# Kernel optimization log

Hardware: AMD Instinct MI355X
Metric: run time of the kernel (lower is better)

## Reference

```python
import jax, jax.numpy as jnp
import numpy as np

NUM_GRAPHS = 256
BN_EPS = 1e-5


def _bn(x, gamma, beta):
    # torch BatchNorm1d training-mode forward: biased batch stats
    m = jnp.mean(x, axis=0)
    v = jnp.mean((x - m) ** 2, axis=0)
    return (x - m) * jax.lax.rsqrt(v + BN_EPS) * gamma + beta


def setup_inputs() -> dict:
    key = jax.random.key(0)
    ks = jax.random.split(key, 12)
    N, D, S = 400000, 128, 64
    h = jax.random.normal(ks[0], (N, D), dtype=jnp.float32)
    sub = jax.random.normal(ks[1], (N, S), dtype=jnp.float32)
    batch = jnp.sort(jax.random.randint(ks[2], (N,), 0, NUM_GRAPHS, dtype=jnp.int32))
    sc = lambda fan_in: 1.0 / np.sqrt(fan_in)
    return {
        "h": h, "sub": sub, "batch": batch,
        # sub_enhance: Linear(S, D) + BN(D) + ReLU
        "W1": jax.random.uniform(ks[3], (S, D), jnp.float32, -sc(S), sc(S)),
        "b1": jnp.zeros((D,), jnp.float32),
        "g1": jnp.ones((D,), jnp.float32),
        "be1": jnp.zeros((D,), jnp.float32),
        # gate: Linear(2D, D) + Sigmoid
        "Wg": jax.random.uniform(ks[4], (2 * D, D), jnp.float32, -sc(2 * D), sc(2 * D)),
        "bg": jnp.zeros((D,), jnp.float32),
        # score_mlp: Linear(2D, D) + BN + ReLU + Linear(D, 1)
        "Ws1": jax.random.uniform(ks[5], (2 * D, D), jnp.float32, -sc(2 * D), sc(2 * D)),
        "bs1": jnp.zeros((D,), jnp.float32),
        "g2": jnp.ones((D,), jnp.float32),
        "be2": jnp.zeros((D,), jnp.float32),
        "Ws2": jax.random.uniform(ks[6], (D, 1), jnp.float32, -sc(D), sc(D)),
        "bs2": jnp.zeros((1,), jnp.float32),
        "mix": jnp.float32(0.5),
    }


def reference(h, sub, batch, W1, b1, g1, be1, Wg, bg, Ws1, bs1, g2, be2, Ws2, bs2, mix):
    G = NUM_GRAPHS
    # counts per graph, guard against empty segments
    counts = jax.ops.segment_sum(jnp.ones_like(batch, jnp.float32), batch, num_segments=G)
    counts = jnp.maximum(counts, 1.0)[:, None]  # [G,1]

    sub_enhanced = jax.nn.relu(_bn(sub @ W1 + b1, g1, be1))  # [N,D]
    gate_weight = jax.nn.sigmoid(jnp.concatenate([h, sub_enhanced], axis=1) @ Wg + bg)
    h_fused = h + gate_weight * sub_enhanced  # [N,D]

    graph_mean = jax.ops.segment_sum(h, batch, num_segments=G) / counts  # [G,D]
    h_sq_mean = jax.ops.segment_sum(h * h, batch, num_segments=G) / counts
    graph_std = jnp.sqrt(jnp.maximum(h_sq_mean - graph_mean ** 2, 1e-8))
    h_dev = (h - graph_mean[batch]) / (graph_std[batch] + 1e-8)  # [N,D]

    z = jax.nn.relu(_bn(jnp.concatenate([h_fused, h_dev], axis=1) @ Ws1 + bs1, g2, be2))
    score_logit = z @ Ws2 + bs2  # [N,1]

    # scatter_softmax over batch segments
    seg_max = jax.ops.segment_max(score_logit, batch, num_segments=G)  # [G,1]
    e = jnp.exp(score_logit - seg_max[batch])
    denom = jax.ops.segment_sum(e, batch, num_segments=G)[batch]
    score = e / denom  # [N,1]

    weighted_fused = jax.ops.segment_sum(h_fused * score, batch, num_segments=G)  # [G,D]
    weighted_orig = graph_mean
    alpha = jax.nn.sigmoid(mix)
    return alpha * weighted_fused + (1.0 - alpha) * weighted_orig
```

## Files before the change

### kernel.cpp

```cpp
#include <hip/hip_runtime.h>

#define DD 128
#define SS 64
#define GG 256
#define LTDA 264
#define LTDS 72

typedef short short8 __attribute__((ext_vector_type(8)));
typedef float f32x4 __attribute__((ext_vector_type(4)));

__device__ __forceinline__ unsigned short f2bf(float x) {
  unsigned u = __float_as_uint(x);
  u += 0x7FFFu + ((u >> 16) & 1u);
  return (unsigned short)(u >> 16);
}
__device__ __forceinline__ float bf2f(unsigned short b) {
  return __uint_as_float(((unsigned)b) << 16);
}
__device__ __forceinline__ unsigned pkbf(float lo, float hi) {
  unsigned r;
  asm("v_cvt_pk_bf16_f32 %0, %1, %2" : "=v"(r) : "v"(lo), "v"(hi));
  return r;
}
__device__ __forceinline__ float fsig(float x) {
  return __builtin_amdgcn_rcpf(1.f + __expf(-x));
}

__device__ __forceinline__ void stage8k(const unsigned short* __restrict__ g,
                                        unsigned short* l, int tid) {
  int wave = tid >> 6;
  const unsigned* gp = (const unsigned*)g;
  unsigned* lp = (unsigned*)l;
  __builtin_amdgcn_global_load_lds(
      (const __attribute__((address_space(1))) unsigned*)(gp + tid * 4),
      (__attribute__((address_space(3))) unsigned*)(lp + wave * 256), 16, 0, 0);
  __builtin_amdgcn_global_load_lds(
      (const __attribute__((address_space(1))) unsigned*)(gp + 1024 + tid * 4),
      (__attribute__((address_space(3))) unsigned*)(lp + 1024 + wave * 256), 16, 0, 0);
}

__device__ __forceinline__ void mfma8(const unsigned short* __restrict__ Abase,
                                      int astride,
                                      const unsigned short* __restrict__ wst,
                                      int k0, int m16, int quad, int mts,
                                      int nts, f32x4 acc[2][4]) {
  short8 af[2];
  af[0] = *(const short8*)(Abase + (size_t)((mts + 0) * 16 + m16) * astride + k0 + quad * 8);
  af[1] = *(const short8*)(Abase + (size_t)((mts + 1) * 16 + m16) * astride + k0 + quad * 8);
  short8 bf[4];
#pragma unroll
  for (int ni = 0; ni < 4; ++ni) {
    int n = (nts + ni) * 16 + m16;
    int s = (quad + (n >> 1)) & 3;
    bf[ni] = *(const short8*)(wst + n * 32 + s * 8);
  }
#pragma unroll
  for (int mi = 0; mi < 2; ++mi)
#pragma unroll
    for (int ni = 0; ni < 4; ++ni)
      acc[mi][ni] = __builtin_amdgcn_mfma_f32_16x16x32_bf16(af[mi], bf[ni],
                                                            acc[mi][ni], 0, 0, 0);
}

__device__ __forceinline__ void mfma8t(const unsigned short* __restrict__ wst,
                                       const unsigned short* __restrict__ Abase,
                                       int k0, int m16, int quad, int mts,
                                       int nts, f32x4 acc[4][2]) {
  short8 wfr[4];
#pragma unroll
  for (int mi = 0; mi < 4; ++mi) {
    int ch = (mts + mi) * 16 + m16;
    int s = (quad + (ch >> 1)) & 3;
    wfr[mi] = *(const short8*)(wst + ch * 32 + s * 8);
  }
  short8 xf[2];
#pragma unroll
  for (int ni = 0; ni < 2; ++ni) {
    int row = (nts + ni) * 16 + m16;
    xf[ni] = *(const short8*)(Abase + (size_t)row * LTDA + k0 + quad * 8);
  }
#pragma unroll
  for (int mi = 0; mi < 4; ++mi)
#pragma unroll
    for (int ni = 0; ni < 2; ++ni)
      acc[mi][ni] = __builtin_amdgcn_mfma_f32_16x16x32_bf16(wfr[mi], xf[ni],
                                                            acc[mi][ni], 0, 0, 0);
}

__global__ void w_prep(const float* __restrict__ W1, const float* __restrict__ Wg,
                       const float* __restrict__ Ws1, unsigned short* __restrict__ w1t,
                       unsigned short* __restrict__ wgt, unsigned short* __restrict__ ws1t) {
  int cb = blockIdx.x;
  const float* W;
  unsigned short* out;
  int kb;
  if (cb < 2) { W = W1; out = w1t; kb = cb; }
  else if (cb < 10) { W = Wg; out = wgt; kb = cb - 2; }
  else { W = Ws1; out = ws1t; kb = cb - 10; }
  out += (size_t)kb * 4096;
  int i = threadIdx.x;
#pragma unroll
  for (int t = 0; t < 2; ++t) {
    int u = i * 2 + t;
    int n = u >> 2, s = u & 3;
    int kc = (s - (n >> 1)) & 3;
    int kbase = kb * 32 + kc * 8;
    unsigned short* o = out + u * 8;
#pragma unroll
    for (int j = 0; j < 8; ++j) o[j] = f2bf(W[(size_t)(kbase + j) * DD + n]);
  }
}

__global__ __launch_bounds__(256, 6) void k1_bn(
    const float* __restrict__ sub, const unsigned short* __restrict__ w1t,
    const float* __restrict__ b1, float* __restrict__ bn1s,
    float* __restrict__ bn1q) {
  __shared__ unsigned short subbuf[64][LTDS];
  __shared__ unsigned short wstage[2][4096];
  __shared__ float bn1l[256];
  int tid = threadIdx.x;
  int row0 = blockIdx.x * 64;
  bn1l[tid] = 0.f;
  for (int i = tid; i < 1024; i += 256) {
    int r = i >> 4, c = (i & 15) * 4;
    float4 v = *(const float4*)&sub[(size_t)(row0 + r) * SS + c];
    uint2 uu;
    uu.x = pkbf(v.x, v.y);
    uu.y = pkbf(v.z, v.w);
    *(uint2*)&subbuf[r][c] = uu;
  }
  stage8k(w1t, &wstage[0][0], tid);
  stage8k(w1t + 4096, &wstage[1][0], tid);
  __syncthreads();
  int lane = tid & 63, wave = tid >> 6;
  int m16 = lane & 15, quad = lane >> 4;
  int mts = 2 * (wave & 1), nts = 4 * (wave >> 1);
  f32x4 acc[2][4];
#pragma unroll
  for (int mi = 0; mi < 2; ++mi)
#pragma unroll
    for (int ni = 0; ni < 4; ++ni) acc[mi][ni] = (f32x4){0.f, 0.f, 0.f, 0.f};
  mfma8(&subbuf[0][0], LTDS, &wstage[0][0], 0, m16, quad, mts, nts, acc);
  mfma8(&subbuf[0][0], LTDS, &wstage[1][0], 32, m16, quad, mts, nts, acc);
#pragma unroll
  for (int ni = 0; ni < 4; ++ni) {
    int col = (nts + ni) * 16 + m16;
    float b1c = b1[col];
    float s = 0.f, q = 0.f;
#pragma unroll
    for (int mi = 0; mi < 2; ++mi)
#pragma unroll
      for (int r = 0; r < 4; ++r) {
        float x = acc[mi][ni][r] + b1c;
        s += x;
        q += x * x;
      }
    s += __shfl_down(s, 32); s += __shfl_down(s, 16);
    q += __shfl_down(q, 32); q += __shfl_down(q, 16);
    if (lane < 16) {
      atomicAdd(&bn1l[col], s);
      atomicAdd(&bn1l[128 + col], q);
    }
  }
  __syncthreads();
  if (tid < 128) {
    atomicAdd(&bn1s[tid], bn1l[tid]);
    atomicAdd(&bn1q[tid], bn1l[128 + tid]);
  }
}

__global__ __launch_bounds__(256, 8) void k1_graph(
    const float* __restrict__ h, const int* __restrict__ batch,
    float* __restrict__ gsum, float* __restrict__ gsq,
    float* __restrict__ counts, int N) {
  __shared__ int bc[256];
  int tid = threadIdx.x;
  int row0 = blockIdx.x * 256;
  {
    int row = row0 + tid;
    bc[tid] = (row < N) ? batch[row] : -1;
  }
  __syncthreads();
  int stripe = tid >> 5, c4 = (tid & 31) * 4;
  float sx = 0, sy = 0, sz = 0, sw = 0, qx = 0, qy = 0, qz = 0, qw = 0, cnt = 0;
  int gcur = -1;
  float4 vbuf[4];
  bool vval[4];
#pragma unroll
  for (int j = 0; j < 4; ++j) {
    int r = stripe + 8 * j;
    vval[j] = bc[r] >= 0;
    if (vval[j]) vbuf[j] = *(const float4*)&h[(size_t)(row0 + r) * DD + c4];
  }
#pragma unroll 1
  for (int mit = 0; mit < 8; ++mit) {
#pragma unroll
    for (int j = 0; j < 4; ++j) {
      int it = mit * 4 + j;
      int r = stripe + 8 * it;
      bool valid = vval[j];
      float4 v = vbuf[j];
      bool nv = (it + 4 < 32) && (bc[r + 32] >= 0);
      vval[j] = nv;
      if (nv) vbuf[j] = *(const float4*)&h[(size_t)(row0 + r + 32) * DD + c4];
      if (valid) {
        int g = bc[r];
        if (g != gcur) {
          if (gcur >= 0) {
            float* gp = &gsum[(size_t)gcur * DD + c4];
            float* qp = &gsq[(size_t)gcur * DD + c4];
            atomicAdd(gp + 0, sx); atomicAdd(gp + 1, sy);
            atomicAdd(gp + 2, sz); atomicAdd(gp + 3, sw);
            atomicAdd(qp + 0, qx); atomicAdd(qp + 1, qy);
            atomicAdd(qp + 2, qz); atomicAdd(qp + 3, qw);
            if ((tid & 31) == 0) atomicAdd(&counts[gcur], cnt);
          }
          gcur = g;
          sx = sy = sz = sw = qx = qy = qz = qw = cnt = 0.f;
        }
        sx += v.x; sy += v.y; sz += v.z; sw += v.w;
        qx = fmaf(v.x, v.x, qx); qy = fmaf(v.y, v.y, qy);
        qz = fmaf(v.z, v.z, qz); qw = fmaf(v.w, v.w, qw);
        cnt += 1.f;
      }
    }
  }
  if (gcur >= 0) {
    float* gp = &gsum[(size_t)gcur * DD + c4];
    float* qp = &gsq[(size_t)gcur * DD + c4];
    atomicAdd(gp + 0, sx); atomicAdd(gp + 1, sy);
    atomicAdd(gp + 2, sz); atomicAdd(gp + 3, sw);
    atomicAdd(qp + 0, qx); atomicAdd(qp + 1, qy);
    atomicAdd(qp + 2, qz); atomicAdd(qp + 3, qw);
    if ((tid & 31) == 0) atomicAdd(&counts[gcur], cnt);
  }
}

__global__ void k2a_bn_final(const float* __restrict__ s, const float* __restrict__ q,
                             const float* __restrict__ gamma, const float* __restrict__ beta,
                             float* __restrict__ sc, float* __restrict__ sh, float Nf) {
  int d = threadIdx.x;
  float m = s[d] / Nf;
  float v = q[d] / Nf - m * m;
  float r = rsqrtf(v + 1e-5f);
  float scv = gamma[d] * r;
  sc[d] = scv;
  sh[d] = beta[d] - m * scv;
}

__global__ void k2_fused(const float* __restrict__ bn1s, const float* __restrict__ bn1q,
                         const float* __restrict__ g1, const float* __restrict__ be1,
                         float* __restrict__ sc1, float* __restrict__ sh1, float Nf,
                         const float* __restrict__ gsum, const float* __restrict__ gsq,
                         const float* __restrict__ counts, float* __restrict__ gmean,
                         float* __restrict__ grstd) {
  int d = threadIdx.x;
  if (blockIdx.x == 0) {
    float m = bn1s[d] / Nf;
    float v = bn1q[d] / Nf - m * m;
    float r = rsqrtf(v + 1e-5f);
    float scv = g1[d] * r;
    sc1[d] = scv;
    sh1[d] = be1[d] - m * scv;
  } else {
    int g = blockIdx.x - 1;
    float c = counts[g];
    float cf = c > 1.f ? c : 1.f;
    size_t idx = (size_t)g * DD + d;
    float m = gsum[idx] / cf;
    float v = gsq[idx] / cf - m * m;
    float sd = sqrtf(fmaxf(v, 1e-8f));
    gmean[idx] = m;
    grstd[idx] = 1.f / (sd + 1e-8f);
  }
}

__global__ __launch_bounds__(256, 3) void k3_main(
    const float* __restrict__ h, const float* __restrict__ sub,
    const int* __restrict__ batch, const unsigned short* __restrict__ w1t,
    const unsigned short* __restrict__ wgt, const unsigned short* __restrict__ ws1t,
    const float* __restrict__ b1, const float* __restrict__ sc1,
    const float* __restrict__ sh1, const float* __restrict__ bg,
    const float* __restrict__ bs1, const float* __restrict__ gmean,
    const float* __restrict__ grstd, float* __restrict__ hfused,
    unsigned short* __restrict__ zp16, float* __restrict__ bn2s,
    float* __restrict__ bn2q, int N) {
  __shared__ unsigned short abuf[64][LTDA];
  __shared__ unsigned short wstage[2][4096];
  __shared__ int bt[64];
  int tid = threadIdx.x;
  int row0 = blockIdx.x * 64;

#pragma unroll
  for (int t = 0; t < 4; ++t) {
    int u = tid + t * 256;
    int r = u >> 4, c8 = (u & 15) * 8;
    const float* hp = &h[(size_t)(row0 + r) * DD + c8];
    float4 v0 = *(const float4*)hp, v1 = *(const float4*)(hp + 4);
    uint4 uu;
    uu.x = pkbf(v0.x, v0.y);
    uu.y = pkbf(v0.z, v0.w);
    uu.z = pkbf(v1.x, v1.y);
    uu.w = pkbf(v1.z, v1.w);
    *(uint4*)&abuf[r][c8] = uu;
  }
#pragma unroll
  for (int t = 0; t < 2; ++t) {
    int u = tid + t * 256;
    int r = u >> 3, c8 = (u & 7) * 8;
    const float* sp = &sub[(size_t)(row0 + r) * SS + c8];
    float4 v0 = *(const float4*)sp, v1 = *(const float4*)(sp + 4);
    uint4 uu;
    uu.x = pkbf(v0.x, v0.y);
    uu.y = pkbf(v0.z, v0.w);
    uu.z = pkbf(v1.x, v1.y);
    uu.w = pkbf(v1.z, v1.w);
    *(uint4*)&abuf[r][128 + c8] = uu;
  }
  if (tid < 64) bt[tid] = batch[row0 + tid];
  stage8k(w1t, &wstage[0][0], tid);
  stage8k(w1t + 4096, &wstage[1][0], tid);
  __syncthreads();

  int lane = tid & 63, wave = tid >> 6;
  int m16 = lane & 15, quad = lane >> 4;
  int mts = 4 * (wave >> 1), nts = 2 * (wave & 1);
  f32x4 acc[4][2];

#pragma unroll
  for (int mi = 0; mi < 4; ++mi)
#pragma unroll
    for (int ni = 0; ni < 2; ++ni) acc[mi][ni] = (f32x4){0.f, 0.f, 0.f, 0.f};
  mfma8t(&wstage[0][0], &abuf[0][0], 128, m16, quad, mts, nts, acc);
  mfma8t(&wstage[1][0], &abuf[0][0], 160, m16, quad, mts, nts, acc);
  __syncthreads();
  stage8k(wgt, &wstage[0][0], tid);
#pragma unroll
  for (int mi = 0; mi < 4; ++mi) {
    int ch0 = (mts + mi) * 16 + quad * 4;
    float4 b1v = *(const float4*)&b1[ch0];
    float4 s1v = *(const float4*)&sc1[ch0];
    float4 h1v = *(const float4*)&sh1[ch0];
#pragma unroll
    for (int ni = 0; ni < 2; ++ni) {
      int row = (nts + ni) * 16 + m16;
      float se0 = fmaxf(fmaf(acc[mi][ni][0] + b1v.x, s1v.x, h1v.x), 0.f);
      float se1 = fmaxf(fmaf(acc[mi][ni][1] + b1v.y, s1v.y, h1v.y), 0.f);
      float se2 = fmaxf(fmaf(acc[mi][ni][2] + b1v.z, s1v.z, h1v.z), 0.f);
      float se3 = fmaxf(fmaf(acc[mi][ni][3] + b1v.w, s1v.w, h1v.w), 0.f);
      uint2 uu;
      uu.x = pkbf(se0, se1);
      uu.y = pkbf(se2, se3);
      *(uint2*)&abuf[row][128 + ch0] = uu;
    }
  }
  __syncthreads();

#pragma unroll
  for (int mi = 0; mi < 4; ++mi)
#pragma unroll
    for (int ni = 0; ni < 2; ++ni) acc[mi][ni] = (f32x4){0.f, 0.f, 0.f, 0.f};
#pragma unroll 1
  for (int c = 0; c < 8; ++c) {
    if (c < 7) stage8k(wgt + (size_t)(c + 1) * 4096, &wstage[(c + 1) & 1][0], tid);
    mfma8t(&wstage[c & 1][0], &abuf[0][0], c * 32, m16, quad, mts, nts, acc);
    __syncthreads();
  }
  stage8k(ws1t, &wstage[0][0], tid);
#pragma unroll
  for (int mi = 0; mi < 4; ++mi) {
    int ch0 = (mts + mi) * 16 + quad * 4;
    float4 bgv = *(const float4*)&bg[ch0];
#pragma unroll
    for (int ni = 0; ni < 2; ++ni) {
      int row = (nts + ni) * 16 + m16;
      int grow = row0 + row;
      float4 hv = *(const float4*)&h[(size_t)grow * DD + ch0];
      uint2 seu = *(const uint2*)&abuf[row][128 + ch0];
      int g = bt[row];
      float4 gm = *(const float4*)&gmean[(size_t)g * DD + ch0];
      float4 gr = *(const float4*)&grstd[(size_t)g * DD + ch0];
      float g0 = fsig(acc[mi][ni][0] + bgv.x);
      float g1v = fsig(acc[mi][ni][1] + bgv.y);
      float g2 = fsig(acc[mi][ni][2] + bgv.z);
      float g3 = fsig(acc[mi][ni][3] + bgv.w);
      float hf0 = fmaf(g0, bf2f((unsigned short)(seu.x & 0xffff)), hv.x);
      float hf1 = fmaf(g1v, bf2f((unsigned short)(seu.x >> 16)), hv.y);
      float hf2 = fmaf(g2, bf2f((unsigned short)(seu.y & 0xffff)), hv.z);
      float hf3 = fmaf(g3, bf2f((unsigned short)(seu.y >> 16)), hv.w);
      float hd0 = (hv.x - gm.x) * gr.x;
      float hd1 = (hv.y - gm.y) * gr.y;
      float hd2 = (hv.z - gm.z) * gr.z;
      float hd3 = (hv.w - gm.w) * gr.w;
      float4 hfv = {hf0, hf1, hf2, hf3};
      *(float4*)&hfused[(size_t)grow * DD + ch0] = hfv;
      uint2 uf, ud;
      uf.x = pkbf(hf0, hf1);
      uf.y = pkbf(hf2, hf3);
      ud.x = pkbf(hd0, hd1);
      ud.y = pkbf(hd2, hd3);
      *(uint2*)&abuf[row][ch0] = uf;
      *(uint2*)&abuf[row][128 + ch0] = ud;
    }
  }
  __syncthreads();

#pragma unroll
  for (int mi = 0; mi < 4; ++mi)
#pragma unroll
    for (int ni = 0; ni < 2; ++ni) acc[mi][ni] = (f32x4){0.f, 0.f, 0.f, 0.f};
#pragma unroll 1
  for (int c = 0; c < 8; ++c) {
    if (c < 7) stage8k(ws1t + (size_t)(c + 1) * 4096, &wstage[(c + 1) & 1][0], tid);
    mfma8t(&wstage[c & 1][0], &abuf[0][0], c * 32, m16, quad, mts, nts, acc);
    __syncthreads();
  }
  float* scr = (float*)&abuf[0][0];
  int srow = (wave & 1) * 16 + m16;
#pragma unroll
  for (int mi = 0; mi < 4; ++mi) {
    int ch0 = (mts + mi) * 16 + quad * 4;
    float4 bsv = *(const float4*)&bs1[ch0];
    f32x4 s4 = (f32x4){0.f, 0.f, 0.f, 0.f};
    f32x4 q4 = (f32x4){0.f, 0.f, 0.f, 0.f};
#pragma unroll
    for (int ni = 0; ni < 2; ++ni) {
      int grow = row0 + (nts + ni) * 16 + m16;
      float z0 = acc[mi][ni][0] + bsv.x;
      float z1 = acc[mi][ni][1] + bsv.y;
      float z2 = acc[mi][ni][2] + bsv.z;
      float z3 = acc[mi][ni][3] + bsv.w;
      uint2 uz;
      uz.x = pkbf(z0, z1);
      uz.y = pkbf(z2, z3);
      *(uint2*)&zp16[(size_t)grow * DD + ch0] = uz;
      s4[0] += z0; s4[1] += z1; s4[2] += z2; s4[3] += z3;
      q4[0] = fmaf(z0, z0, q4[0]); q4[1] = fmaf(z1, z1, q4[1]);
      q4[2] = fmaf(z2, z2, q4[2]); q4[3] = fmaf(z3, z3, q4[3]);
    }
    *(f32x4*)&scr[srow * 132 + ch0] = s4;
    *(f32x4*)&scr[4224 + srow * 132 + ch0] = q4;
  }
  __syncthreads();
  if (tid < 128) {
    float s = 0.f, q = 0.f;
#pragma unroll 4
    for (int i = 0; i < 32; ++i) {
      s += scr[i * 132 + tid];
      q += scr[4224 + i * 132 + tid];
    }
    atomicAdd(&bn2s[tid], s);
    atomicAdd(&bn2q[tid], q);
  }
}

__global__ __launch_bounds__(256, 6) void k56_score(
    const unsigned short* __restrict__ zp16, const float* __restrict__ hf,
    const int* __restrict__ batch, const float* __restrict__ sc2,
    const float* __restrict__ sh2, const float* __restrict__ Ws2,
    const float* __restrict__ bs2, float* __restrict__ denom,
    float* __restrict__ wf, int N) {
  __shared__ int bc[256];
  int tid = threadIdx.x;
  int row0 = blockIdx.x * 256;
  {
    int row = row0 + tid;
    bc[tid] = (row < N) ? batch[row] : -1;
  }
  __syncthreads();
  int stripe = tid >> 5, c4 = (tid & 31) * 4;
  float4 s2 = *(const float4*)&sc2[c4];
  float4 h2 = *(const float4*)&sh2[c4];
  float4 w2 = *(const float4*)&Ws2[c4];
  float b2 = bs2[0];
  float ax = 0, ay = 0, az = 0, aw = 0, ds = 0;
  int gcur = -1;
  uint2 vz[4];
  float4 vh[4];
  bool vval[4];
#pragma unroll
  for (int j = 0; j < 4; ++j) {
    int r = stripe + 8 * j;
    vval[j] = bc[r] >= 0;
    if (vval[j]) {
      vz[j] = *(const uint2*)&zp16[(size_t)(row0 + r) * DD + c4];
      vh[j] = *(const float4*)&hf[(size_t)(row0 + r) * DD + c4];
    }
  }
#pragma unroll 1
  for (int mit = 0; mit < 8; ++mit) {
#pragma unroll
    for (int j = 0; j < 4; ++j) {
      int it = mit * 4 + j;
      int r = stripe + 8 * it;
      bool valid = vval[j];
      uint2 z2v = vz[j];
      float4 hv = vh[j];
      bool nv = (it + 4 < 32) && (bc[r + 32] >= 0);
      vval[j] = nv;
      if (nv) {
        vz[j] = *(const uint2*)&zp16[(size_t)(row0 + r + 32) * DD + c4];
        vh[j] = *(const float4*)&hf[(size_t)(row0 + r + 32) * DD + c4];
      }
      if (valid) {
        int g = bc[r];
        if (g != gcur) {
          if (gcur >= 0) {
            float* wp = &wf[(size_t)gcur * DD + c4];
            atomicAdd(wp + 0, ax); atomicAdd(wp + 1, ay);
            atomicAdd(wp + 2, az); atomicAdd(wp + 3, aw);
            if ((tid & 31) == 0) atomicAdd(&denom[gcur], ds);
          }
          gcur = g;
          ax = ay = az = aw = ds = 0.f;
        }
        float z0 = bf2f((unsigned short)(z2v.x & 0xffff));
        float z1 = bf2f((unsigned short)(z2v.x >> 16));
        float zz2 = bf2f((unsigned short)(z2v.y & 0xffff));
        float z3 = bf2f((unsigned short)(z2v.y >> 16));
        float p = fmaxf(fmaf(z0, s2.x, h2.x), 0.f) * w2.x;
        p = fmaf(fmaxf(fmaf(z1, s2.y, h2.y), 0.f), w2.y, p);
        p = fmaf(fmaxf(fmaf(zz2, s2.z, h2.z), 0.f), w2.z, p);
        p = fmaf(fmaxf(fmaf(z3, s2.w, h2.w), 0.f), w2.w, p);
        p += __shfl_xor(p, 16); p += __shfl_xor(p, 8);
        p += __shfl_xor(p, 4);  p += __shfl_xor(p, 2);
        p += __shfl_xor(p, 1);
        float e = __expf(p + b2);
        ax = fmaf(hv.x, e, ax); ay = fmaf(hv.y, e, ay);
        az = fmaf(hv.z, e, az); aw = fmaf(hv.w, e, aw);
        ds += e;
      }
    }
  }
  if (gcur >= 0) {
    float* wp = &wf[(size_t)gcur * DD + c4];
    atomicAdd(wp + 0, ax); atomicAdd(wp + 1, ay);
    atomicAdd(wp + 2, az); atomicAdd(wp + 3, aw);
    if ((tid & 31) == 0) atomicAdd(&denom[gcur], ds);
  }
}

__global__ void k7_out(const float* __restrict__ wf, const float* __restrict__ denom,
                       const float* __restrict__ gmean, const float* __restrict__ mix,
                       float* __restrict__ out) {
  int g = blockIdx.x, d = threadIdx.x;
  float alpha = 1.f / (1.f + expf(-mix[0]));
  float dn = denom[g];
  size_t idx = (size_t)g * DD + d;
  float w = (dn > 0.f) ? wf[idx] / dn : 0.f;
  out[idx] = alpha * w + (1.f - alpha) * gmean[idx];
}

extern "C" void kernel_launch(void* const* d_in, const int* in_sizes, int n_in,
                              void* d_out, int out_size, void* d_ws, size_t ws_size,
                              hipStream_t stream) {
  const float* h   = (const float*)d_in[0];
  const float* sub = (const float*)d_in[1];
  const int* batch = (const int*)d_in[2];
  const float* W1  = (const float*)d_in[3];
  const float* b1  = (const float*)d_in[4];
  const float* g1  = (const float*)d_in[5];
  const float* be1 = (const float*)d_in[6];
  const float* Wg  = (const float*)d_in[7];
  const float* bg  = (const float*)d_in[8];
  const float* Ws1 = (const float*)d_in[9];
  const float* bs1 = (const float*)d_in[10];
  const float* g2  = (const float*)d_in[11];
  const float* be2 = (const float*)d_in[12];
  const float* Ws2 = (const float*)d_in[13];
  const float* bs2 = (const float*)d_in[14];
  const float* mix = (const float*)d_in[15];
  float* out = (float*)d_out;
  const int N = in_sizes[0] / DD;
  const int nB1 = N / 64;
  const int nBG = (N + 255) / 256;

  float* ws = (float*)d_ws;
  size_t off = 0;
  float* hf    = ws + off; off += (size_t)N * DD;
  unsigned short* zp16 = (unsigned short*)(ws + off); off += (size_t)N * DD / 2;
  float* zbase = ws + off;
  float* gsum  = ws + off; off += (size_t)GG * DD;
  float* gsq   = ws + off; off += (size_t)GG * DD;
  float* wf    = ws + off; off += (size_t)GG * DD;
  float* bn1s  = ws + off; off += 128;
  float* bn1q  = ws + off; off += 128;
  float* bn2s  = ws + off; off += 128;
  float* bn2q  = ws + off; off += 128;
  float* counts = ws + off; off += GG;
  float* denom  = ws + off; off += GG;
  size_t zcount = (size_t)(ws + off - zbase);
  float* gmean = ws + off; off += (size_t)GG * DD;
  float* grstd = ws + off; off += (size_t)GG * DD;
  float* sc1 = ws + off; off += 128;
  float* sh1 = ws + off; off += 128;
  float* sc2 = ws + off; off += 128;
  float* sh2 = ws + off; off += 128;
  unsigned short* w1t  = (unsigned short*)(ws + off); off += 8192 / 2;
  unsigned short* wgt  = (unsigned short*)(ws + off); off += 32768 / 2;
  unsigned short* ws1t = (unsigned short*)(ws + off); off += 32768 / 2;

  hipMemsetAsync(zbase, 0, zcount * sizeof(float), stream);
  w_prep<<<18, 256, 0, stream>>>(W1, Wg, Ws1, w1t, wgt, ws1t);

  k1_bn<<<nB1, 256, 0, stream>>>(sub, w1t, b1, bn1s, bn1q);
  k1_graph<<<nBG, 256, 0, stream>>>(h, batch, gsum, gsq, counts, N);
  k2_fused<<<1 + GG, 128, 0, stream>>>(bn1s, bn1q, g1, be1, sc1, sh1, (float)N,
                                       gsum, gsq, counts, gmean, grstd);

  k3_main<<<nB1, 256, 0, stream>>>(h, sub, batch, w1t, wgt, ws1t, b1, sc1, sh1,
                                   bg, bs1, gmean, grstd, hf, zp16, bn2s, bn2q, N);

  k2a_bn_final<<<1, 128, 0, stream>>>(bn2s, bn2q, g2, be2, sc2, sh2, (float)N);
  k56_score<<<nBG, 256, 0, stream>>>(zp16, hf, batch, sc2, sh2, Ws2, bs2,
                                     denom, wf, N);
  k7_out<<<GG, 128, 0, stream>>>(wf, denom, gmean, mix, out);
}
```

Measured before the change: 898.6 us.

## Merge BN1 and graph-stat kernels and replicate BN accumulators to cut atomic contention

Folds the sub-projection BN-statistics kernel and the per-graph h statistics kernel into one launch. Block IDs are interleaved so every fifth block does graph reduction and the rest do the MFMA BN1 pass, letting the memory-bound h scan overlap with the compute-bound GEMM. Both BN1 and BN2 column sums now go into 64 replicated partial buffers indexed by block ID, and the finalize kernels reduce them. This is meant to lower same-address atomic contention, at the cost of a larger memset and a lower launch-bounds occupancy hint for the fused kernel.

```diff
diff --git a/kernel.cpp b/kernel.cpp
--- a/kernel.cpp
+++ b/kernel.cpp
@@ -3,6 +3,7 @@
 #define DD 128
 #define SS 64
 #define GG 256
+#define NREP 64
 #define LTDA 264
 #define LTDS 72
 
@@ -111,15 +112,86 @@
   }
 }
 
-__global__ __launch_bounds__(256, 6) void k1_bn(
+__global__ __launch_bounds__(256, 4) void k1_fused(
     const float* __restrict__ sub, const unsigned short* __restrict__ w1t,
-    const float* __restrict__ b1, float* __restrict__ bn1s,
-    float* __restrict__ bn1q) {
+    const float* __restrict__ b1, float* __restrict__ bn1p,
+    const float* __restrict__ h, const int* __restrict__ batch,
+    float* __restrict__ gsum, float* __restrict__ gsq,
+    float* __restrict__ counts, int N, int nBG) {
   __shared__ unsigned short subbuf[64][LTDS];
   __shared__ unsigned short wstage[2][4096];
   __shared__ float bn1l[256];
   int tid = threadIdx.x;
-  int row0 = blockIdx.x * 64;
+  int bid = blockIdx.x;
+  int g5 = bid / 5, r5 = bid - g5 * 5;
+  bool isGraph = (r5 == 0) && (g5 < nBG);
+
+  if (isGraph) {
+    int* bc = (int*)bn1l;
+    int row0 = g5 * 256;
+    {
+      int row = row0 + tid;
+      bc[tid] = (row < N) ? batch[row] : -1;
+    }
+    __syncthreads();
+    int stripe = tid >> 5, c4 = (tid & 31) * 4;
+    float sx = 0, sy = 0, sz = 0, sw = 0, qx = 0, qy = 0, qz = 0, qw = 0, cnt = 0;
+    int gcur = -1;
+    float4 vbuf[4];
+    bool vval[4];
+#pragma unroll
+    for (int j = 0; j < 4; ++j) {
+      int r = stripe + 8 * j;
+      vval[j] = bc[r] >= 0;
+      if (vval[j]) vbuf[j] = *(const float4*)&h[(size_t)(row0 + r) * DD + c4];
+    }
+#pragma unroll 1
+    for (int mit = 0; mit < 8; ++mit) {
+#pragma unroll
+      for (int j = 0; j < 4; ++j) {
+        int it = mit * 4 + j;
+        int r = stripe + 8 * it;
+        bool valid = vval[j];
+        float4 v = vbuf[j];
+        bool nv = (it + 4 < 32) && (bc[r + 32] >= 0);
+        vval[j] = nv;
+        if (nv) vbuf[j] = *(const float4*)&h[(size_t)(row0 + r + 32) * DD + c4];
+        if (valid) {
+          int g = bc[r];
+          if (g != gcur) {
+            if (gcur >= 0) {
+              float* gp = &gsum[(size_t)gcur * DD + c4];
+              float* qp = &gsq[(size_t)gcur * DD + c4];
+              atomicAdd(gp + 0, sx); atomicAdd(gp + 1, sy);
+              atomicAdd(gp + 2, sz); atomicAdd(gp + 3, sw);
+              atomicAdd(qp + 0, qx); atomicAdd(qp + 1, qy);
+              atomicAdd(qp + 2, qz); atomicAdd(qp + 3, qw);
+              if ((tid & 31) == 0) atomicAdd(&counts[gcur], cnt);
+            }
+            gcur = g;
+            sx = sy = sz = sw = qx = qy = qz = qw = cnt = 0.f;
+          }
+          sx += v.x; sy += v.y; sz += v.z; sw += v.w;
+          qx = fmaf(v.x, v.x, qx); qy = fmaf(v.y, v.y, qy);
+          qz = fmaf(v.z, v.z, qz); qw = fmaf(v.w, v.w, qw);
+          cnt += 1.f;
+        }
+      }
+    }
+    if (gcur >= 0) {
+      float* gp = &gsum[(size_t)gcur * DD + c4];
+      float* qp = &gsq[(size_t)gcur * DD + c4];
+      atomicAdd(gp + 0, sx); atomicAdd(gp + 1, sy);
+      atomicAdd(gp + 2, sz); atomicAdd(gp + 3, sw);
+      atomicAdd(qp + 0, qx); atomicAdd(qp + 1, qy);
+      atomicAdd(qp + 2, qz); atomicAdd(qp + 3, qw);
+      if ((tid & 31) == 0) atomicAdd(&counts[gcur], cnt);
+    }
+    return;
+  }
+
+  int nbefore = (g5 + 1 < nBG) ? (g5 + 1) : nBG;
+  int row0 = (bid - nbefore) * 64;
   bn1l[tid] = 0.f;
   for (int i = tid; i < 1024; i += 256) {
     int r = i >> 4, c = (i & 15) * 4;
@@ -163,92 +235,28 @@
     }
   }
   __syncthreads();
-  if (tid < 128) {
-    atomicAdd(&bn1s[tid], bn1l[tid]);
-    atomicAdd(&bn1q[tid], bn1l[128 + tid]);
-  }
-}
-
-__global__ __launch_bounds__(256, 8) void k1_graph(
-    const float* __restrict__ h, const int* __restrict__ batch,
-    float* __restrict__ gsum, float* __restrict__ gsq,
-    float* __restrict__ counts, int N) {
-  __shared__ int bc[256];
-  int tid = threadIdx.x;
-  int row0 = blockIdx.x * 256;
-  {
-    int row = row0 + tid;
-    bc[tid] = (row < N) ? batch[row] : -1;
-  }
-  __syncthreads();
-  int stripe = tid >> 5, c4 = (tid & 31) * 4;
-  float sx = 0, sy = 0, sz = 0, sw = 0, qx = 0, qy = 0, qz = 0, qw = 0, cnt = 0;
-  int gcur = -1;
-  float4 vbuf[4];
-  bool vval[4];
-#pragma unroll
-  for (int j = 0; j < 4; ++j) {
-    int r = stripe + 8 * j;
-    vval[j] = bc[r] >= 0;
-    if (vval[j]) vbuf[j] = *(const float4*)&h[(size_t)(row0 + r) * DD + c4];
-  }
-#pragma unroll 1
-  for (int mit = 0; mit < 8; ++mit) {
-#pragma unroll
-    for (int j = 0; j < 4; ++j) {
-      int it = mit * 4 + j;
-      int r = stripe + 8 * it;
-      bool valid = vval[j];
-      float4 v = vbuf[j];
-      bool nv = (it + 4 < 32) && (bc[r + 32] >= 0);
-      vval[j] = nv;
-      if (nv) vbuf[j] = *(const float4*)&h[(size_t)(row0 + r + 32) * DD + c4];
-      if (valid) {
-        int g = bc[r];
-        if (g != gcur) {
-          if (gcur >= 0) {
-            float* gp = &gsum[(size_t)gcur * DD + c4];
-            float* qp = &gsq[(size_t)gcur * DD + c4];
-            atomicAdd(gp + 0, sx); atomicAdd(gp + 1, sy);
-            atomicAdd(gp + 2, sz); atomicAdd(gp + 3, sw);
-            atomicAdd(qp + 0, qx); atomicAdd(qp + 1, qy);
-            atomicAdd(qp + 2, qz); atomicAdd(qp + 3, qw);
-            if ((tid & 31) == 0) atomicAdd(&counts[gcur], cnt);
-          }
-          gcur = g;
-          sx = sy = sz = sw = qx = qy = qz = qw = cnt = 0.f;
-        }
-        sx += v.x; sy += v.y; sz += v.z; sw += v.w;
-        qx = fmaf(v.x, v.x, qx); qy = fmaf(v.y, v.y, qy);
-        qz = fmaf(v.z, v.z, qz); qw = fmaf(v.w, v.w, qw);
-        cnt += 1.f;
-      }
-    }
-  }
-  if (gcur >= 0) {
-    float* gp = &gsum[(size_t)gcur * DD + c4];
-    float* qp = &gsq[(size_t)gcur * DD + c4];
-    atomicAdd(gp + 0, sx); atomicAdd(gp + 1, sy);
-    atomicAdd(gp + 2, sz); atomicAdd(gp + 3, sw);
-    atomicAdd(qp + 0, qx); atomicAdd(qp + 1, qy);
-    atomicAdd(qp + 2, qz); atomicAdd(qp + 3, qw);
-    if ((tid & 31) == 0) atomicAdd(&counts[gcur], cnt);
-  }
-}
-
-__global__ void k2a_bn_final(const float* __restrict__ s, const float* __restrict__ q,
+  atomicAdd(&bn1p[(size_t)(bid & (NREP - 1)) * 256 + tid], bn1l[tid]);
+}
+
+__global__ void k2a_bn_final(const float* __restrict__ bn2p,
                              const float* __restrict__ gamma, const float* __restrict__ beta,
                              float* __restrict__ sc, float* __restrict__ sh, float Nf) {
   int d = threadIdx.x;
-  float m = s[d] / Nf;
-  float v = q[d] / Nf - m * m;
-  float r = rsqrtf(v + 1e-5f);
-  float scv = gamma[d] * r;
+  float s = 0.f, q = 0.f;
+#pragma unroll 4
+  for (int r = 0; r < NREP; ++r) {
+    s += bn2p[r * 256 + d];
+    q += bn2p[r * 256 + 128 + d];
+  }
+  float m = s / Nf;
+  float v = q / Nf - m * m;
+  float rr = rsqrtf(v + 1e-5f);
+  float scv = gamma[d] * rr;
   sc[d] = scv;
   sh[d] = beta[d] - m * scv;
 }
 
-__global__ void k2_fused(const float* __restrict__ bn1s, const float* __restrict__ bn1q,
+__global__ void k2_fused(const float* __restrict__ bn1p,
                          const float* __restrict__ g1, const float* __restrict__ be1,
                          float* __restrict__ sc1, float* __restrict__ sh1, float Nf,
                          const float* __restrict__ gsum, const float* __restrict__ gsq,
@@ -256,10 +264,16 @@
                          float* __restrict__ grstd) {
   int d = threadIdx.x;
   if (blockIdx.x == 0) {
-    float m = bn1s[d] / Nf;
-    float v = bn1q[d] / Nf - m * m;
-    float r = rsqrtf(v + 1e-5f);
-    float scv = g1[d] * r;
+    float s = 0.f, q = 0.f;
+#pragma unroll 4
+    for (int r = 0; r < NREP; ++r) {
+      s += bn1p[r * 256 + d];
+      q += bn1p[r * 256 + 128 + d];
+    }
+    float m = s / Nf;
+    float v = q / Nf - m * m;
+    float rr = rsqrtf(v + 1e-5f);
+    float scv = g1[d] * rr;
     sc1[d] = scv;
     sh1[d] = be1[d] - m * scv;
   } else {
@@ -283,8 +297,7 @@
     const float* __restrict__ sh1, const float* __restrict__ bg,
     const float* __restrict__ bs1, const float* __restrict__ gmean,
     const float* __restrict__ grstd, float* __restrict__ hfused,
-    unsigned short* __restrict__ zp16, float* __restrict__ bn2s,
-    float* __restrict__ bn2q, int N) {
+    unsigned short* __restrict__ zp16, float* __restrict__ bn2p, int N) {
   __shared__ unsigned short abuf[64][LTDA];
   __shared__ unsigned short wstage[2][4096];
   __shared__ int bt[64];
@@ -449,8 +462,9 @@
       s += scr[i * 132 + tid];
       q += scr[4224 + i * 132 + tid];
     }
-    atomicAdd(&bn2s[tid], s);
-    atomicAdd(&bn2q[tid], q);
+    float* rp = &bn2p[(size_t)(blockIdx.x & (NREP - 1)) * 256];
+    atomicAdd(&rp[tid], s);
+    atomicAdd(&rp[128 + tid], q);
   }
 }
 
@@ -583,10 +597,8 @@
   float* gsum  = ws + off; off += (size_t)GG * DD;
   float* gsq   = ws + off; off += (size_t)GG * DD;
   float* wf    = ws + off; off += (size_t)GG * DD;
-  float* bn1s  = ws + off; off += 128;
-  float* bn1q  = ws + off; off += 128;
-  float* bn2s  = ws + off; off += 128;
-  float* bn2q  = ws + off; off += 128;
+  float* bn1p  = ws + off; off += (size_t)NREP * 256;
+  float* bn2p  = ws + off; off += (size_t)NREP * 256;
   float* counts = ws + off; off += GG;
   float* denom  = ws + off; off += GG;
   size_t zcount = (size_t)(ws + off - zbase);
@@ -603,15 +615,15 @@
   hipMemsetAsync(zbase, 0, zcount * sizeof(float), stream);
   w_prep<<<18, 256, 0, stream>>>(W1, Wg, Ws1, w1t, wgt, ws1t);
 
-  k1_bn<<<nB1, 256, 0, stream>>>(sub, w1t, b1, bn1s, bn1q);
-  k1_graph<<<nBG, 256, 0, stream>>>(h, batch, gsum, gsq, counts, N);
-  k2_fused<<<1 + GG, 128, 0, stream>>>(bn1s, bn1q, g1, be1, sc1, sh1, (float)N,
+  k1_fused<<<nB1 + nBG, 256, 0, stream>>>(sub, w1t, b1, bn1p,
+                                          h, batch, gsum, gsq, counts, N, nBG);
+  k2_fused<<<1 + GG, 128, 0, stream>>>(bn1p, g1, be1, sc1, sh1, (float)N,
                                        gsum, gsq, counts, gmean, grstd);
 
   k3_main<<<nB1, 256, 0, stream>>>(h, sub, batch, w1t, wgt, ws1t, b1, sc1, sh1,
-                                   bg, bs1, gmean, grstd, hf, zp16, bn2s, bn2q, N);
-
-  k2a_bn_final<<<1, 128, 0, stream>>>(bn2s, bn2q, g2, be2, sc2, sh2, (float)N);
+                                   bg, bs1, gmean, grstd, hf, zp16, bn2p, N);
+
+  k2a_bn_final<<<1, 128, 0, stream>>>(bn2p, g2, be2, sc2, sh2, (float)N);
   k56_score<<<nBG, 256, 0, stream>>>(zp16, hf, batch, sc2, sh2, Ws2, bs2,
                                      denom, wf, N);
   k7_out<<<GG, 128, 0, stream>>>(wf, denom, gmean, mix, out);
```

New measurement: 747.8 us. 16.8% less time.
